# Performance work log

Hardware: AMD Instinct MI355X
Metric: run time of the kernel (lower is better)

## Reference

```python
import jax, jax.numpy as jnp
import numpy as np

NUM_ENTITIES = 100000
NUM_RELATIONS = 500
DIM = 512
CHANNELS = 32
KERNEL = 3
BATCH = 2048


def setup_inputs() -> dict:
    key = jax.random.key(0)
    ks = jax.random.split(key, 9)
    # xavier_uniform bounds
    b_ent = float(np.sqrt(6.0 / (NUM_ENTITIES + DIM)))
    b_rel = float(np.sqrt(6.0 / (NUM_RELATIONS + DIM)))
    ent = jax.random.uniform(ks[0], (NUM_ENTITIES, DIM), jnp.float32, -b_ent, b_ent)
    rel = jax.random.uniform(ks[1], (NUM_RELATIONS, DIM), jnp.float32, -b_rel, b_rel)
    # Conv1d(1, CHANNELS, KERNEL) default init: U(-s, s), s = 1/sqrt(in_ch*k)
    s_conv = float(1.0 / np.sqrt(1 * KERNEL))
    conv_w = jax.random.uniform(ks[2], (CHANNELS, 1, KERNEL), jnp.float32, -s_conv, s_conv)
    conv_b = jax.random.uniform(ks[3], (CHANNELS,), jnp.float32, -s_conv, s_conv)
    # Linear(CHANNELS*DIM, DIM)
    s_proj = float(1.0 / np.sqrt(CHANNELS * DIM))
    proj_w = jax.random.uniform(ks[4], (DIM, CHANNELS * DIM), jnp.float32, -s_proj, s_proj)
    proj_b = jax.random.uniform(ks[5], (DIM,), jnp.float32, -s_proj, s_proj)
    h = jax.random.randint(ks[6], (BATCH,), 0, NUM_ENTITIES, jnp.int32)
    r = jax.random.randint(ks[7], (BATCH,), 0, NUM_RELATIONS, jnp.int32)
    t = jax.random.randint(ks[8], (BATCH,), 0, NUM_ENTITIES, jnp.int32)
    return {"h": h, "r": r, "t": t, "ent": ent, "rel": rel,
            "conv_w": conv_w, "conv_b": conv_b, "proj_w": proj_w, "proj_b": proj_b}


def reference(h, r, t, ent, rel, conv_w, conv_b, proj_w, proj_b):
    dim = ent.shape[1]
    h_e = ent[h]                                   # [B, D]
    r_e = rel[r]                                   # [B, D]
    x = jnp.concatenate([h_e, r_e], axis=-1)[:, None, :]   # [B, 1, 2D]
    x = jax.lax.conv_general_dilated(
        x, conv_w, window_strides=(1,), padding='SAME',
        dimension_numbers=('NCH', 'OIH', 'NCH'))   # [B, C, 2D]
    x = jax.nn.relu(x + conv_b[None, :, None])
    x = x[..., :dim]                               # [B, C, D]
    x = x.reshape(x.shape[0], -1)                  # [B, C*D]
    x = x @ proj_w.T + proj_b                      # [B, D]
    scores = x @ ent.T                             # [B, N] full-entity scores
    return scores[jnp.arange(t.shape[0]), t]       # [B]
```

## Files before the change

### kernel.cpp

```cpp
#include <hip/hip_runtime.h>

#define DIM    512
#define CH     32
#define KDIM   16384
#define BATCH  2048
#define NOUT   512
#define PWN    (NOUT * KDIM)

#define BM 128
#define BN 128
#define BK 32
#define KSPLIT 8
#define KC (KDIM / KSPLIT)

typedef short bf16x8 __attribute__((ext_vector_type(8)));
typedef float f32x4  __attribute__((ext_vector_type(4)));

__device__ __forceinline__ float b2f(unsigned short u) {
    union { unsigned int i; float f; } v; v.i = ((unsigned int)u) << 16; return v.f;
}
__device__ __forceinline__ unsigned short f2b(float f) {
    union { float f; unsigned int i; } v; v.f = f;
    unsigned int r = v.i + 0x7fffu + ((v.i >> 16) & 1u);
    return (unsigned short)(r >> 16);
}
__device__ __forceinline__ float ldv(const void* p, size_t i, int isf) {
    return isf ? ((const float*)p)[i] : b2f(((const unsigned short*)p)[i]);
}
__device__ __forceinline__ int sniff_isf32(const unsigned short* ent_raw) {
    int lane = threadIdx.x & 63;
    unsigned short u = ent_raw[2 * lane];
    int eb = (u >> 8) & 0x7F;
    unsigned long long m = __ballot(eb >= 0x36 && eb < 0x3C);
    return (__popcll(m) < 32) ? 1 : 0;
}

__device__ __forceinline__ void gload_lds16(const unsigned short* g, unsigned short* l) {
    __builtin_amdgcn_global_load_lds(
        (const __attribute__((address_space(1))) void*)g,
        (__attribute__((address_space(3))) void*)l,
        16, 0, 0);
}

__global__ __launch_bounds__(256) void convert_kernel(
    const void* __restrict__ projw, unsigned short* __restrict__ pw16,
    const unsigned short* __restrict__ ent_raw) {
    const int isf = sniff_isf32(ent_raw);
    size_t i0 = ((size_t)blockIdx.x * 256 + threadIdx.x) * 4;
    if (i0 >= PWN) return;
    if (isf) {
        f32x4 v = *(const f32x4*)((const float*)projw + i0);
        unsigned int p0 = (unsigned int)f2b(v[0]) | ((unsigned int)f2b(v[1]) << 16);
        unsigned int p1 = (unsigned int)f2b(v[2]) | ((unsigned int)f2b(v[3]) << 16);
        *(unsigned int*)(pw16 + i0) = p0;
        *(unsigned int*)(pw16 + i0 + 2) = p1;
    } else {
        *(unsigned long long*)(pw16 + i0) =
            *(const unsigned long long*)((const unsigned short*)projw + i0);
    }
}

__global__ __launch_bounds__(256) void feat_kernel(
    const int* __restrict__ h, const int* __restrict__ r,
    const void* __restrict__ ent, const void* __restrict__ rel,
    const void* __restrict__ conv_w, const void* __restrict__ conv_b,
    unsigned short* __restrict__ feat)
{
    __shared__ float xs[DIM + 2];
    __shared__ float wS[CH][4];
    const int b   = blockIdx.x;
    const int tid = threadIdx.x;
    const int isf = sniff_isf32((const unsigned short*)ent);

    const size_t hb = (size_t)h[b] * DIM;
    for (int j = tid; j < DIM; j += 256) xs[1 + j] = ldv(ent, hb + j, isf);
    if (tid == 0) xs[0] = 0.0f;
    if (tid == 1) xs[DIM + 1] = ldv(rel, (size_t)r[b] * DIM, isf);
    if (tid >= 64 && tid < 96) {
        int c = tid - 64;
        wS[c][0] = ldv(conv_w, c * 3 + 0, isf);
        wS[c][1] = ldv(conv_w, c * 3 + 1, isf);
        wS[c][2] = ldv(conv_w, c * 3 + 2, isf);
        wS[c][3] = ldv(conv_b, c, isf);
    }
    __syncthreads();

    unsigned short* fb = feat + (size_t)b * KDIM;
    const int i0 = tid * 2;
    float x0 = xs[i0], x1 = xs[i0 + 1], x2 = xs[i0 + 2], x3 = xs[i0 + 3];
    #pragma unroll 8
    for (int c = 0; c < CH; ++c) {
        float w0 = wS[c][0], w1 = wS[c][1], w2 = wS[c][2], cb = wS[c][3];
        float v0 = fmaxf(fmaf(w0, x0, fmaf(w1, x1, fmaf(w2, x2, cb))), 0.0f);
        float v1 = fmaxf(fmaf(w0, x1, fmaf(w1, x2, fmaf(w2, x3, cb))), 0.0f);
        unsigned int pack = (unsigned int)f2b(v0) | ((unsigned int)f2b(v1) << 16);
        *(unsigned int*)&fb[c * DIM + i0] = pack;
    }
}

__global__ __launch_bounds__(256, 2) void gemm_kernel(
    const unsigned short* __restrict__ feat,
    const unsigned short* __restrict__ pw16,
    float* __restrict__ Xp)
{
    __shared__ __align__(16) unsigned short As[BM * BK];
    __shared__ __align__(16) unsigned short Bs[BN * BK];

    const int tid  = threadIdx.x;
    const int lane = tid & 63;
    const int wave = tid >> 6;
    const int wm = wave & 1;
    const int wn = wave >> 1;
    const int bx = blockIdx.x, by = blockIdx.y, bz = blockIdx.z;

    const unsigned short* Ab = feat + (size_t)(bx * BM) * KDIM + bz * KC;
    const unsigned short* Bb = pw16 + (size_t)(by * BN) * KDIM + bz * KC;

    const int row_ld = tid >> 2;
    const int koff   = (tid & 3) * 8;

    const f32x4 zero = {0.f, 0.f, 0.f, 0.f};
    f32x4 acc[4][4];
    #pragma unroll
    for (int i = 0; i < 4; ++i)
        #pragma unroll
        for (int j = 0; j < 4; ++j) acc[i][j] = zero;

    const int fRow = lane & 15;
    const int fK   = (lane >> 4) * 8;

    for (int kk = 0; kk < KC; kk += BK) {
        gload_lds16(Ab + (size_t)row_ld * KDIM + kk + koff,        As + row_ld * BK + koff);
        gload_lds16(Ab + (size_t)(row_ld + 64) * KDIM + kk + koff, As + (row_ld + 64) * BK + koff);
        gload_lds16(Bb + (size_t)row_ld * KDIM + kk + koff,        Bs + row_ld * BK + koff);
        gload_lds16(Bb + (size_t)(row_ld + 64) * KDIM + kk + koff, Bs + (row_ld + 64) * BK + koff);
        __syncthreads();

        bf16x8 af[4], bfr[4];
        #pragma unroll
        for (int mi = 0; mi < 4; ++mi)
            af[mi] = *(const bf16x8*)&As[(wm * 64 + mi * 16 + fRow) * BK + fK];
        #pragma unroll
        for (int ni = 0; ni < 4; ++ni)
            bfr[ni] = *(const bf16x8*)&Bs[(wn * 64 + ni * 16 + fRow) * BK + fK];
        #pragma unroll
        for (int mi = 0; mi < 4; ++mi)
            #pragma unroll
            for (int ni = 0; ni < 4; ++ni)
                acc[mi][ni] = __builtin_amdgcn_mfma_f32_16x16x32_bf16(
                    af[mi], bfr[ni], acc[mi][ni], 0, 0, 0);
        __syncthreads();
    }

    float* Xs = Xp + (size_t)bz * BATCH * NOUT;
    const int rbase = bx * BM + wm * 64 + (lane >> 4) * 4;
    const int cbase = by * BN + wn * 64 + (lane & 15);
    #pragma unroll
    for (int mi = 0; mi < 4; ++mi)
        #pragma unroll
        for (int ni = 0; ni < 4; ++ni)
            #pragma unroll
            for (int rr = 0; rr < 4; ++rr) {
                int row = rbase + mi * 16 + rr;
                int col = cbase + ni * 16;
                Xs[(size_t)row * NOUT + col] = acc[mi][ni][rr];
            }
}

__global__ __launch_bounds__(256) void score_kernel(
    const int* __restrict__ t, const void* __restrict__ ent,
    const float* __restrict__ Xp, const void* __restrict__ projb,
    void* __restrict__ out)
{
    const int lane = threadIdx.x & 63;
    const int wave = threadIdx.x >> 6;
    const int b = blockIdx.x * 4 + wave;
    const int isf = sniff_isf32((const unsigned short*)ent);
    const size_t tb = (size_t)t[b] * DIM;
    float s = 0.f;
    #pragma unroll
    for (int j = 0; j < 8; ++j) {
        int d = lane + 64 * j;
        float xp = ldv(projb, d, isf);
        #pragma unroll
        for (int z = 0; z < KSPLIT; ++z)
            xp += Xp[(size_t)z * BATCH * NOUT + (size_t)b * NOUT + d];
        s += xp * ldv(ent, tb + d, isf);
    }
    #pragma unroll
    for (int o = 32; o; o >>= 1) s += __shfl_xor(s, o, 64);
    if (lane == 0) {
        if (isf) ((float*)out)[b] = s;
        else     ((unsigned short*)out)[b] = f2b(s);
    }
}

extern "C" void kernel_launch(void* const* d_in, const int* in_sizes, int n_in,
                              void* d_out, int out_size, void* d_ws, size_t ws_size,
                              hipStream_t stream)
{
    const int* h = (const int*)d_in[0];
    const int* r = (const int*)d_in[1];
    const int* t = (const int*)d_in[2];
    const void* ent    = d_in[3];
    const void* rel    = d_in[4];
    const void* conv_w = d_in[5];
    const void* conv_b = d_in[6];
    const void* projw  = d_in[7];
    const void* projb  = d_in[8];

    unsigned short* feat = (unsigned short*)d_ws;
    unsigned short* pw16 = (unsigned short*)((char*)d_ws + (size_t)BATCH * KDIM * 2);
    float* Xp = (float*)((char*)pw16 + (size_t)PWN * 2);

    convert_kernel<<<(PWN / 4 + 255) / 256, 256, 0, stream>>>(projw, pw16, (const unsigned short*)ent);
    feat_kernel<<<BATCH, 256, 0, stream>>>(h, r, ent, rel, conv_w, conv_b, feat);
    gemm_kernel<<<dim3(BATCH / BM, NOUT / BN, KSPLIT), 256, 0, stream>>>(feat, pw16, Xp);
    score_kernel<<<BATCH / 4, 256, 0, stream>>>(t, ent, Xp, projb, d_out);
}
```

Before: 336.4 us.

## Merge convert and feature kernels, double GEMM K-tile, vectorize score loads

Folds the weight bf16 conversion and the conv feature kernel into one launch by splitting the grid into conversion blocks and feature blocks. Doubles the GEMM K tile to 64, so each iteration issues twice the loads and MFMAs per barrier pair and the loop has half as many iterations. Vectorizes the score kernel's fp32 path with float4 loads of the partial sums, bias and target embedding. The changes aim to cut launch overhead and synchronization, at the cost of doubled LDS for the GEMM and a larger kernel.

```diff
diff --git a/kernel.cpp b/kernel.cpp
--- a/kernel.cpp
+++ b/kernel.cpp
@@ -6,10 +6,11 @@
 #define BATCH  2048
 #define NOUT   512
 #define PWN    (NOUT * KDIM)
+#define CONVBLK (PWN / 4 / 256)
 
 #define BM 128
 #define BN 128
-#define BK 32
+#define BK 64
 #define KSPLIT 8
 #define KC (KDIM / KSPLIT)
 
@@ -42,35 +43,34 @@
         16, 0, 0);
 }
 
-__global__ __launch_bounds__(256) void convert_kernel(
-    const void* __restrict__ projw, unsigned short* __restrict__ pw16,
-    const unsigned short* __restrict__ ent_raw) {
-    const int isf = sniff_isf32(ent_raw);
-    size_t i0 = ((size_t)blockIdx.x * 256 + threadIdx.x) * 4;
-    if (i0 >= PWN) return;
-    if (isf) {
-        f32x4 v = *(const f32x4*)((const float*)projw + i0);
-        unsigned int p0 = (unsigned int)f2b(v[0]) | ((unsigned int)f2b(v[1]) << 16);
-        unsigned int p1 = (unsigned int)f2b(v[2]) | ((unsigned int)f2b(v[3]) << 16);
-        *(unsigned int*)(pw16 + i0) = p0;
-        *(unsigned int*)(pw16 + i0 + 2) = p1;
-    } else {
-        *(unsigned long long*)(pw16 + i0) =
-            *(const unsigned long long*)((const unsigned short*)projw + i0);
-    }
-}
-
-__global__ __launch_bounds__(256) void feat_kernel(
+__global__ __launch_bounds__(256) void prep_kernel(
     const int* __restrict__ h, const int* __restrict__ r,
     const void* __restrict__ ent, const void* __restrict__ rel,
     const void* __restrict__ conv_w, const void* __restrict__ conv_b,
-    unsigned short* __restrict__ feat)
-{
+    const void* __restrict__ projw,
+    unsigned short* __restrict__ pw16, unsigned short* __restrict__ feat)
+{
+    const int tid = threadIdx.x;
+    const int isf = sniff_isf32((const unsigned short*)ent);
+
+    if (blockIdx.x < CONVBLK) {
+        size_t i0 = ((size_t)blockIdx.x * 256 + tid) * 4;
+        if (isf) {
+            f32x4 v = *(const f32x4*)((const float*)projw + i0);
+            unsigned int p0 = (unsigned int)f2b(v[0]) | ((unsigned int)f2b(v[1]) << 16);
+            unsigned int p1 = (unsigned int)f2b(v[2]) | ((unsigned int)f2b(v[3]) << 16);
+            *(unsigned int*)(pw16 + i0) = p0;
+            *(unsigned int*)(pw16 + i0 + 2) = p1;
+        } else {
+            *(unsigned long long*)(pw16 + i0) =
+                *(const unsigned long long*)((const unsigned short*)projw + i0);
+        }
+        return;
+    }
+
     __shared__ float xs[DIM + 2];
     __shared__ float wS[CH][4];
-    const int b   = blockIdx.x;
-    const int tid = threadIdx.x;
-    const int isf = sniff_isf32((const unsigned short*)ent);
+    const int b = blockIdx.x - CONVBLK;
 
     const size_t hb = (size_t)h[b] * DIM;
     for (int j = tid; j < DIM; j += 256) xs[1 + j] = ldv(ent, hb + j, isf);
@@ -116,8 +116,8 @@
     const unsigned short* Ab = feat + (size_t)(bx * BM) * KDIM + bz * KC;
     const unsigned short* Bb = pw16 + (size_t)(by * BN) * KDIM + bz * KC;
 
-    const int row_ld = tid >> 2;
-    const int koff   = (tid & 3) * 8;
+    const int row_ld = tid >> 3;
+    const int koff   = (tid & 7) * 8;
 
     const f32x4 zero = {0.f, 0.f, 0.f, 0.f};
     f32x4 acc[4][4];
@@ -130,25 +130,30 @@
     const int fK   = (lane >> 4) * 8;
 
     for (int kk = 0; kk < KC; kk += BK) {
-        gload_lds16(Ab + (size_t)row_ld * KDIM + kk + koff,        As + row_ld * BK + koff);
-        gload_lds16(Ab + (size_t)(row_ld + 64) * KDIM + kk + koff, As + (row_ld + 64) * BK + koff);
-        gload_lds16(Bb + (size_t)row_ld * KDIM + kk + koff,        Bs + row_ld * BK + koff);
-        gload_lds16(Bb + (size_t)(row_ld + 64) * KDIM + kk + koff, Bs + (row_ld + 64) * BK + koff);
+        #pragma unroll
+        for (int j = 0; j < 4; ++j) {
+            int rw = row_ld + 32 * j;
+            gload_lds16(Ab + (size_t)rw * KDIM + kk + koff, As + rw * BK + koff);
+            gload_lds16(Bb + (size_t)rw * KDIM + kk + koff, Bs + rw * BK + koff);
+        }
         __syncthreads();
 
-        bf16x8 af[4], bfr[4];
-        #pragma unroll
-        for (int mi = 0; mi < 4; ++mi)
-            af[mi] = *(const bf16x8*)&As[(wm * 64 + mi * 16 + fRow) * BK + fK];
-        #pragma unroll
-        for (int ni = 0; ni < 4; ++ni)
-            bfr[ni] = *(const bf16x8*)&Bs[(wn * 64 + ni * 16 + fRow) * BK + fK];
-        #pragma unroll
-        for (int mi = 0; mi < 4; ++mi)
+        #pragma unroll
+        for (int ko = 0; ko < 2; ++ko) {
+            bf16x8 af[4], bfr[4];
+            #pragma unroll
+            for (int mi = 0; mi < 4; ++mi)
+                af[mi] = *(const bf16x8*)&As[(wm * 64 + mi * 16 + fRow) * BK + ko * 32 + fK];
             #pragma unroll
             for (int ni = 0; ni < 4; ++ni)
-                acc[mi][ni] = __builtin_amdgcn_mfma_f32_16x16x32_bf16(
-                    af[mi], bfr[ni], acc[mi][ni], 0, 0, 0);
+                bfr[ni] = *(const bf16x8*)&Bs[(wn * 64 + ni * 16 + fRow) * BK + ko * 32 + fK];
+            #pragma unroll
+            for (int mi = 0; mi < 4; ++mi)
+                #pragma unroll
+                for (int ni = 0; ni < 4; ++ni)
+                    acc[mi][ni] = __builtin_amdgcn_mfma_f32_16x16x32_bf16(
+                        af[mi], bfr[ni], acc[mi][ni], 0, 0, 0);
+        }
         __syncthreads();
     }
 
@@ -178,14 +183,30 @@
     const int isf = sniff_isf32((const unsigned short*)ent);
     const size_t tb = (size_t)t[b] * DIM;
     float s = 0.f;
-    #pragma unroll
-    for (int j = 0; j < 8; ++j) {
-        int d = lane + 64 * j;
-        float xp = ldv(projb, d, isf);
-        #pragma unroll
-        for (int z = 0; z < KSPLIT; ++z)
-            xp += Xp[(size_t)z * BATCH * NOUT + (size_t)b * NOUT + d];
-        s += xp * ldv(ent, tb + d, isf);
+    if (isf) {
+        const float* te = (const float*)ent + tb;
+        const float* pb = (const float*)projb;
+        const int d0 = lane * 8;
+        #pragma unroll
+        for (int jj = 0; jj < 2; ++jj) {
+            int d = d0 + jj * 4;
+            f32x4 xp = *(const f32x4*)(pb + d);
+            #pragma unroll
+            for (int z = 0; z < KSPLIT; ++z)
+                xp += *(const f32x4*)(Xp + (size_t)z * BATCH * NOUT + (size_t)b * NOUT + d);
+            f32x4 tv = *(const f32x4*)(te + d);
+            s += xp[0]*tv[0] + xp[1]*tv[1] + xp[2]*tv[2] + xp[3]*tv[3];
+        }
+    } else {
+        #pragma unroll
+        for (int j = 0; j < 8; ++j) {
+            int d = lane + 64 * j;
+            float xp = ldv(projb, d, 0);
+            #pragma unroll
+            for (int z = 0; z < KSPLIT; ++z)
+                xp += Xp[(size_t)z * BATCH * NOUT + (size_t)b * NOUT + d];
+            s += xp * ldv(ent, tb + d, 0);
+        }
     }
     #pragma unroll
     for (int o = 32; o; o >>= 1) s += __shfl_xor(s, o, 64);
@@ -213,8 +234,8 @@
     unsigned short* pw16 = (unsigned short*)((char*)d_ws + (size_t)BATCH * KDIM * 2);
     float* Xp = (float*)((char*)pw16 + (size_t)PWN * 2);
 
-    convert_kernel<<<(PWN / 4 + 255) / 256, 256, 0, stream>>>(projw, pw16, (const unsigned short*)ent);
-    feat_kernel<<<BATCH, 256, 0, stream>>>(h, r, ent, rel, conv_w, conv_b, feat);
+    prep_kernel<<<CONVBLK + BATCH, 256, 0, stream>>>(h, r, ent, rel, conv_w, conv_b,
+                                                     projw, pw16, feat);
     gemm_kernel<<<dim3(BATCH / BM, NOUT / BN, KSPLIT), 256, 0, stream>>>(feat, pw16, Xp);
     score_kernel<<<BATCH / 4, 256, 0, stream>>>(t, ent, Xp, projb, d_out);
 }
```

Result: no change. 334.1 us, median of 2 (-0.7%).
